# Kernel optimization log

Measured on AMD Instinct MI355X. Metric: run time of the kernel, lower is better.

Reference implementation:

```python
import jax, jax.numpy as jnp
import numpy as np

B, N = 2, 2048
DIM, NH, DH = 640, 10, 64
DINNER = 2560
L = 4
DEMB = 32
NTOKS = [128, 64]
NFEAT = 19
FDIM = 280
FEATD = DIM - DEMB * len(NTOKS)  # 576
SQRTD = float(np.sqrt(DH))


def _ln(x, g, b, eps=1e-5):
    m = jnp.mean(x, -1, keepdims=True)
    v = jnp.var(x, -1, keepdims=True)
    return (x - m) * jax.lax.rsqrt(v + eps) * g + b


def setup_inputs() -> dict:
    key = jax.random.key(0)
    ks = iter(jax.random.split(key, 32))
    s = 0.05
    return {
        "x_feats": jax.random.normal(next(ks), (B, N, NFEAT), jnp.float32),
        "x_toks": jax.random.randint(next(ks), (B, N, 2), 0, 64),
        "mask": jnp.ones((B, N), jnp.float32),
        "emb0": jax.random.normal(next(ks), (NTOKS[0] + 1, DEMB)) * s,
        "emb1": jax.random.normal(next(ks), (NTOKS[1] + 1, DEMB)) * s,
        "feat_w": jax.random.normal(next(ks), (FEATD, NFEAT)) * s,
        "feat_b": jnp.zeros((FEATD,)),
        "qkv_w": jax.random.normal(next(ks), (L, 3 * DIM, DIM)) * s,
        "qkv_b": jnp.zeros((L, 3 * DIM)),
        "o_w": jax.random.normal(next(ks), (L, DIM, DIM)) * s,
        "ln1_g": jnp.ones((L, DIM)), "ln1_b": jnp.zeros((L, DIM)),
        "ln2_g": jnp.ones((L, DIM)), "ln2_b": jnp.zeros((L, DIM)),
        "p1_w": jax.random.normal(next(ks), (L, DINNER, DIM)) * s,
        "p1_b": jnp.zeros((L, DINNER)),
        "p2_w": jax.random.normal(next(ks), (L, DIM, DINNER)) * s,
        "p2_b": jnp.zeros((L, DIM)),
        "fn_g": jnp.ones((DIM,)), "fn_b": jnp.zeros((DIM,)),
        "lin1_w": jax.random.normal(next(ks), (FDIM, DIM)) * s,
        "lin1_b": jnp.zeros((FDIM,)),
        "rb1_w": jax.random.normal(next(ks), (FDIM, FDIM)) * s,
        "rb1_b": jnp.zeros((FDIM,)),
        "rb2_w": jax.random.normal(next(ks), (FDIM, FDIM)) * s,
        "rb2_b": jnp.zeros((FDIM,)),
        "out_w": jax.random.normal(next(ks), (1, FDIM)) * s,
        "out_b": jnp.zeros((1,)),
    }


def _forward(x_feats, x_toks, mask, emb0, emb1, feat_w, feat_b,
             qkv_w, qkv_b, o_w, ln1_g, ln1_b, ln2_g, ln2_b,
             p1_w, p1_b, p2_w, p2_b, fn_g, fn_b,
             lin1_w, lin1_b, rb1_w, rb1_b, rb2_w, rb2_b, out_w, out_b):
    # mask outer product [B,N,N]; additive mask 0 where allowed, -1e20 elsewhere
    mask2 = jnp.einsum('bi,bj->bij', mask, mask)
    add_mask = jnp.where(mask2 > 0, 0.0, -1e20)

    # embeddings + feature projection -> [B,N,DIM]
    Z = jnp.concatenate([emb0[x_toks[..., 0]], emb1[x_toks[..., 1]],
                         x_feats @ feat_w.T + feat_b], axis=-1)

    def layer(Z, prm):
        qw, qb, ow, g1, b1, g2, b2, w1, c1, w2, c2 = prm
        inp = Z
        Zn = _ln(Z, g1, b1)
        # qkv reshaped to [B,N,H,3*DH], chunked along last dim: V, Q, K
        qkv = (Zn @ qw.T + qb).reshape(B, N, NH, 3 * DH)
        V, Q, K = qkv[..., :DH], qkv[..., DH:2 * DH], qkv[..., 2 * DH:]
        W = jnp.einsum('bnhd,bmhd->bhnm', Q, K) / SQRTD + add_mask[:, None]
        W = jax.nn.softmax(W, axis=3) * mask2[:, None]  # post-softmax mult mask
        attn = jnp.einsum('bhnm,bmhd->bnhd', W, V).reshape(B, N, DIM)
        Z = jax.nn.leaky_relu(attn) @ ow.T + inp  # leaky_relu BEFORE o_net
        inp = Z
        Zn = _ln(Z, g2, b2)
        Z = jax.nn.relu(Zn @ w1.T + c1) @ w2.T + c2 + inp
        return Z, None

    Z, _ = jax.lax.scan(layer, Z,
                        (qkv_w, qkv_b, o_w, ln1_g, ln1_b, ln2_g, ln2_b,
                         p1_w, p1_b, p2_w, p2_b))
    Z = _ln(Z, fn_g, fn_b)
    # ranking head: 1x1 convs == per-token linears
    h = Z @ lin1_w.T + lin1_b
    h = h + (jax.nn.relu(h @ rb1_w.T + rb1_b) @ rb2_w.T + rb2_b)
    return (h @ out_w.T + out_b)[..., 0]  # [B,N]


def reference(x_feats, x_toks, mask, emb0, emb1, feat_w, feat_b,
              qkv_w, qkv_b, o_w, ln1_g, ln1_b, ln2_g, ln2_b,
              p1_w, p1_b, p2_w, p2_b, fn_g, fn_b,
              lin1_w, lin1_b, rb1_w, rb1_b, rb2_w, rb2_b, out_w, out_b):
    return _forward(x_feats, x_toks, mask, emb0, emb1, feat_w, feat_b,
                    qkv_w, qkv_b, o_w, ln1_g, ln1_b, ln2_g, ln2_b,
                    p1_w, p1_b, p2_w, p2_b, fn_g, fn_b,
                    lin1_w, lin1_b, rb1_w, rb1_b, rb2_w, rb2_b, out_w, out_b)
```

## Files before the change

### kernel.cpp

```cpp
#include <hip/hip_runtime.h>

#define B_ 2
#define N_ 2048
#define DIM_ 640
#define NH_ 10
#define DH_ 64
#define DINNER_ 2560
#define L_ 4
#define FDIM_ 280
#define FDIMP_ 320
#define FEATD_ 576
#define NFEAT_ 19
#define ROWS_ (B_*N_)
#define NSPLIT_ 4
#define NITS_ 8

typedef __attribute__((ext_vector_type(8))) unsigned short ushort8;
typedef __attribute__((ext_vector_type(8))) __bf16 bf16x8;
typedef __attribute__((ext_vector_type(4))) __bf16 bf16x4;
typedef __attribute__((ext_vector_type(4))) float f32x4;
typedef __attribute__((ext_vector_type(2))) unsigned int u32x2;

static __device__ __forceinline__ unsigned short f2bf(float f){
  unsigned int u = __builtin_bit_cast(unsigned int, f);
  u += 0x7fffu + ((u >> 16) & 1u);
  return (unsigned short)(u >> 16);
}

static __device__ __forceinline__ f32x4 mfma16(ushort8 a, ushort8 b, f32x4 c){
  return __builtin_amdgcn_mfma_f32_16x16x32_bf16(
      __builtin_bit_cast(bf16x8, a), __builtin_bit_cast(bf16x8, b), c, 0, 0, 0);
}

#define GLD(src,dst) __builtin_amdgcn_global_load_lds((const __attribute__((address_space(1))) void*)(src), (__attribute__((address_space(3))) void*)(dst), 16, 0, 0)

#define SEG0 4915200
#define SEG1 1638400
#define SEG2 6553600
#define SEG3 6553600
#define SEG4 179200
#define SEG5 89600
#define SEG6 89600
#define SEG7 655360
#define SEG8 655360
#define SEG9 4096
#define E0 SEG0
#define E9 (SEG0+SEG1+SEG2+SEG3+SEG4+SEG5+SEG6+SEG7+SEG8+SEG9)

__global__ __launch_bounds__(256) void prep_kernel(
    const float* __restrict__ qkv_w, const float* __restrict__ o_w,
    const float* __restrict__ p1_w, const float* __restrict__ p2_w,
    const float* __restrict__ lin1_w, const float* __restrict__ rb1_w,
    const float* __restrict__ rb2_w, const float* __restrict__ mask,
    unsigned short* __restrict__ qkvw, unsigned short* __restrict__ oww,
    unsigned short* __restrict__ p1w, unsigned short* __restrict__ p2w,
    unsigned short* __restrict__ l1w, unsigned short* __restrict__ r1w,
    unsigned short* __restrict__ r2w, unsigned int* __restrict__ hb1z,
    unsigned int* __restrict__ hb2z, float* __restrict__ mbb)
{
  for (int i = blockIdx.x*256 + threadIdx.x; i < E9; i += gridDim.x*256){
    int j = i;
    if (j < E0) { qkvw[j] = f2bf(qkv_w[j]); continue; }
    j -= E0;
    if (j < SEG1) { oww[j] = f2bf(o_w[j]); continue; }
    j -= SEG1;
    if (j < SEG2) { p1w[j] = f2bf(p1_w[j]); continue; }
    j -= SEG2;
    if (j < SEG3) { p2w[j] = f2bf(p2_w[j]); continue; }
    j -= SEG3;
    if (j < SEG4) { l1w[j] = f2bf(lin1_w[j]); continue; }
    j -= SEG4;
    if (j < SEG5) { int r = j/FDIMP_, c = j - r*FDIMP_;
                    r1w[j] = (c<FDIM_) ? f2bf(rb1_w[r*FDIM_+c]) : (unsigned short)0; continue; }
    j -= SEG5;
    if (j < SEG6) { int r = j/FDIMP_, c = j - r*FDIMP_;
                    r2w[j] = (c<FDIM_) ? f2bf(rb2_w[r*FDIM_+c]) : (unsigned short)0; continue; }
    j -= SEG6;
    if (j < SEG7) { hb1z[j] = 0u; continue; }
    j -= SEG7;
    if (j < SEG8) { hb2z[j] = 0u; continue; }
    j -= SEG8;
    mbb[j] = (mask[j] > 0.f) ? 0.f : -1e30f;
  }
}

__global__ __launch_bounds__(256) void embed_kernel(const float* __restrict__ xf,
    const int* __restrict__ xt, const float* __restrict__ e0, const float* __restrict__ e1,
    const float* __restrict__ fw, const float* __restrict__ fb, float* __restrict__ Z){
  int row = blockIdx.x;
  __shared__ float f[NFEAT_];
  int t = threadIdx.x;
  if (t < NFEAT_) f[t] = xf[row*NFEAT_ + t];
  __syncthreads();
  if (t < 32) {
    int tok0 = xt[row*2];
    Z[(size_t)row*DIM_ + t] = e0[tok0*32 + t];
  } else if (t < 64) {
    int tok1 = xt[row*2+1];
    Z[(size_t)row*DIM_ + t] = e1[tok1*32 + (t-32)];
  }
  for (int fo = t; fo < FEATD_; fo += 256){
    float acc = fb[fo];
    #pragma unroll
    for (int k=0;k<NFEAT_;k++) acc += f[k]*fw[fo*NFEAT_+k];
    Z[(size_t)row*DIM_ + 64 + fo] = acc;
  }
}

__global__ __launch_bounds__(256) void ln_kernel(const float* __restrict__ X,
    const float* __restrict__ g, const float* __restrict__ bb,
    unsigned short* __restrict__ out){
  int lane = threadIdx.x & 63;
  int row = blockIdx.x*4 + (threadIdx.x >> 6);
  const float* x = X + (size_t)row*DIM_;
  float v[10]; float s=0.f, sq=0.f;
  #pragma unroll
  for (int j=0;j<10;j++){ float t = x[lane + j*64]; v[j]=t; s+=t; sq+=t*t; }
  #pragma unroll
  for (int off=1; off<64; off<<=1){ s += __shfl_xor(s, off, 64); sq += __shfl_xor(sq, off, 64); }
  float mean = s*(1.f/DIM_);
  float var = sq*(1.f/DIM_) - mean*mean;
  float rstd = rsqrtf(var + 1e-5f);
  unsigned short* o = out + (size_t)row*DIM_;
  #pragma unroll
  for (int j=0;j<10;j++){ int c = lane + j*64; o[c] = f2bf((v[j]-mean)*rstd*g[c] + bb[c]); }
}

template<bool BIAS, bool RELU, bool RES, bool OUTF, bool OUTB>
__global__ __launch_bounds__(256) void gemm_kernel(
    const unsigned short* __restrict__ A, int lda,
    const unsigned short* __restrict__ Bw, int ldb,
    const float* __restrict__ bias,
    const float* __restrict__ Res, int ldres,
    float* __restrict__ Cf, int ldcf,
    unsigned short* __restrict__ Cb, int ldcb,
    int Ncols, int K)
{
  __shared__ __align__(128) unsigned short As[2][8192];
  __shared__ __align__(128) unsigned short Bs[2][8192];
  int t = threadIdx.x;
  int wid = t >> 6, lane = t & 63;
  int wr = wid >> 1, wc = wid & 1;
  int lg = lane >> 4, lm = lane & 15;
  int orig = blockIdx.y*gridDim.x + blockIdx.x;
  int nwg = gridDim.x*gridDim.y;
  int wg = ((orig & 7) * (nwg >> 3)) + (orig >> 3);
  int bx = wg % gridDim.x, by = wg / gridDim.x;
  int row0 = by * 128;
  int col0 = bx * 128;

  const unsigned short* aSrc[4];
  const unsigned short* bSrc[4];
  #pragma unroll
  for (int j=0;j<4;j++){
    int s = t + j*256;
    int r = s >> 3;
    int c = (s & 7) ^ (((r >> 2) & 1) << 1);
    aSrc[j] = A + (size_t)(row0 + r)*lda + c*8;
    int br = col0 + r; if (br >= Ncols) br = Ncols - 1;
    bSrc[j] = Bw + (size_t)br*ldb + c*8;
  }

  f32x4 acc[4][4];
  #pragma unroll
  for (int m=0;m<4;m++)
    #pragma unroll
    for (int n=0;n<4;n++) acc[m][n] = f32x4{0.f,0.f,0.f,0.f};

  int nk = K >> 6;
  #pragma unroll
  for (int j=0;j<4;j++){
    GLD(aSrc[j], &As[0][(t + j*256)*8]);
    GLD(bSrc[j], &Bs[0][(t + j*256)*8]);
  }

  int swz = (lm & 4) >> 1;
  for (int tk=0; tk<nk; ++tk){
    int cur = tk & 1;
    if (tk+1 < nk){
      int kt = (tk+1) << 6;
      #pragma unroll
      for (int j=0;j<4;j++){
        GLD(aSrc[j]+kt, &As[cur^1][(t + j*256)*8]);
        GLD(bSrc[j]+kt, &Bs[cur^1][(t + j*256)*8]);
      }
      asm volatile("s_waitcnt vmcnt(8)" ::: "memory");
    } else {
      asm volatile("s_waitcnt vmcnt(0)" ::: "memory");
    }
    __builtin_amdgcn_s_barrier();
    asm volatile("" ::: "memory");
    const unsigned short* Ac = &As[cur][0];
    const unsigned short* Bc = &Bs[cur][0];
    #pragma unroll
    for (int kk=0;kk<2;kk++){
      int ch = ((kk*4 + lg) ^ swz) * 8;
      ushort8 af[4], bfr[4];
      #pragma unroll
      for (int m=0;m<4;m++) af[m] = *(const ushort8*)(Ac + (wr*64 + m*16 + lm)*64 + ch);
      #pragma unroll
      for (int n=0;n<4;n++) bfr[n] = *(const ushort8*)(Bc + (wc*64 + n*16 + lm)*64 + ch);
      #pragma unroll
      for (int m=0;m<4;m++)
        #pragma unroll
        for (int n=0;n<4;n++)
          acc[m][n] = mfma16(af[m], bfr[n], acc[m][n]);
    }
    asm volatile("" ::: "memory");
    __builtin_amdgcn_s_barrier();
  }

  #pragma unroll
  for (int m=0;m<4;m++){
    int rbase = row0 + wr*64 + m*16 + lg*4;
    #pragma unroll
    for (int n=0;n<4;n++){
      int cc = col0 + wc*64 + n*16 + lm;
      if (cc < Ncols){
        float bv = 0.f;
        if (BIAS) bv = bias[cc];
        #pragma unroll
        for (int rr=0;rr<4;rr++){
          float v = acc[m][n][rr] + bv;
          if (RELU) v = fmaxf(v, 0.f);
          if (RES) v += Res[(size_t)(rbase+rr)*ldres + cc];
          if (OUTF) Cf[(size_t)(rbase+rr)*ldcf + cc] = v;
          if (OUTB) Cb[(size_t)(rbase+rr)*ldcb + cc] = f2bf(v);
        }
      }
    }
  }
}

template<bool BIAS, bool RELU, bool RES, bool OUTF, bool OUTB>
__global__ __launch_bounds__(256) void gemm64_kernel(
    const unsigned short* __restrict__ A, int lda,
    const unsigned short* __restrict__ Bw, int ldb,
    const float* __restrict__ bias,
    const float* __restrict__ Res, int ldres,
    float* __restrict__ Cf, int ldcf,
    unsigned short* __restrict__ Cb, int ldcb,
    int Ncols, int K)
{
  __shared__ __align__(128) unsigned short As[2][64*64];
  __shared__ __align__(128) unsigned short Bs[2][64*64];
  int t = threadIdx.x;
  int wid = t >> 6, lane = t & 63;
  int wr = wid >> 1, wc = wid & 1;
  int lg = lane >> 4, lm = lane & 15;
  int orig = blockIdx.y*gridDim.x + blockIdx.x;
  int nwg = gridDim.x*gridDim.y;
  int wg = ((orig & 7) * (nwg >> 3)) + (orig >> 3);
  int bx = wg % gridDim.x, by = wg / gridDim.x;
  int row0 = by * 64;
  int col0 = bx * 64;

  int ar0 = t >> 3;
  int ar1 = ar0 + 32;
  int aq = (t & 7) ^ (((ar0 >> 2) & 1) << 1);
  const unsigned short* a0 = A + (size_t)(row0+ar0)*lda + aq*8;
  const unsigned short* a1 = A + (size_t)(row0+ar1)*lda + aq*8;
  int br0 = col0+ar0; if (br0 >= Ncols) br0 = Ncols-1;
  int br1 = col0+ar1; if (br1 >= Ncols) br1 = Ncols-1;
  const unsigned short* b0 = Bw + (size_t)br0*ldb + aq*8;
  const unsigned short* b1 = Bw + (size_t)br1*ldb + aq*8;
  int l0 = t*8, l1 = (t+256)*8;

  f32x4 acc[2][2];
  #pragma unroll
  for (int m=0;m<2;m++)
    #pragma unroll
    for (int n=0;n<2;n++) acc[m][n] = f32x4{0.f,0.f,0.f,0.f};

  int nk = K >> 6;
  GLD(a0, &As[0][l0]); GLD(b0, &Bs[0][l0]);
  GLD(a1, &As[0][l1]); GLD(b1, &Bs[0][l1]);

  int swz = (lm & 4) >> 1;
  for (int tk=0; tk<nk; ++tk){
    int cur = tk & 1;
    if (tk+1 < nk){
      int koff = (tk+1) << 6;
      GLD(a0+koff, &As[cur^1][l0]); GLD(b0+koff, &Bs[cur^1][l0]);
      GLD(a1+koff, &As[cur^1][l1]); GLD(b1+koff, &Bs[cur^1][l1]);
      asm volatile("s_waitcnt vmcnt(4)" ::: "memory");
    } else {
      asm volatile("s_waitcnt vmcnt(0)" ::: "memory");
    }
    __builtin_amdgcn_s_barrier();
    asm volatile("" ::: "memory");
    const unsigned short* Ac = &As[cur][0];
    const unsigned short* Bc = &Bs[cur][0];
    #pragma unroll
    for (int kk=0;kk<2;kk++){
      int ch = ((kk*4 + lg) ^ swz) * 8;
      ushort8 af[2], bfr[2];
      #pragma unroll
      for (int m=0;m<2;m++) af[m] = *(const ushort8*)(Ac + (wr*32 + m*16 + lm)*64 + ch);
      #pragma unroll
      for (int n=0;n<2;n++) bfr[n] = *(const ushort8*)(Bc + (wc*32 + n*16 + lm)*64 + ch);
      #pragma unroll
      for (int m=0;m<2;m++)
        #pragma unroll
        for (int n=0;n<2;n++)
          acc[m][n] = mfma16(af[m], bfr[n], acc[m][n]);
    }
    asm volatile("" ::: "memory");
    __builtin_amdgcn_s_barrier();
  }

  #pragma unroll
  for (int m=0;m<2;m++){
    int rbase = row0 + wr*32 + m*16 + lg*4;
    #pragma unroll
    for (int n=0;n<2;n++){
      int cc = col0 + wc*32 + n*16 + lm;
      if (cc < Ncols){
        float bv = 0.f;
        if (BIAS) bv = bias[cc];
        #pragma unroll
        for (int rr=0;rr<4;rr++){
          float v = acc[m][n][rr] + bv;
          if (RELU) v = fmaxf(v, 0.f);
          if (RES) v += Res[(size_t)(rbase+rr)*ldres + cc];
          if (OUTF) Cf[(size_t)(rbase+rr)*ldcf + cc] = v;
          if (OUTB) Cb[(size_t)(rbase+rr)*ldcb + cc] = f2bf(v);
        }
      }
    }
  }
}

__global__ __launch_bounds__(256) void attn_kernel(const unsigned short* __restrict__ qkv,
    const float* __restrict__ mb, unsigned short* __restrict__ op, float* __restrict__ lpp){
  int bh = blockIdx.y; int b = bh/NH_, h = bh%NH_;
  int t = threadIdx.x; int wid = t>>6, lane = t&63, lg = lane>>4, lm = lane&15;
  int q0 = blockIdx.x*64 + wid*16;
  int it0 = blockIdx.z * NITS_;
  size_t prow = (size_t)blockIdx.z*ROWS_ + b*N_;

  __shared__ __align__(128) unsigned short Ks[2][4096];
  __shared__ __align__(128) unsigned short Vs[2][4096];
  __shared__ __align__(16) float maskL[NITS_*64];

  const size_t base = (size_t)b*N_*1920 + (size_t)h*192;
  const size_t kvoff = (size_t)it0*64*1920;

  int c0 = t, c1 = t+256;
  int kk0 = c0>>3, kc0 = (c0&7)^(kk0&7);
  int kk1 = c1>>3, kc1 = (c1&7)^(kk1&7);
  const unsigned short* kS0 = qkv + base + kvoff + 128 + (size_t)kk0*1920 + kc0*8;
  const unsigned short* kS1 = qkv + base + kvoff + 128 + (size_t)kk1*1920 + kc1*8;
  int vk0 = ((c0>>5)<<2)|((c0>>1)&3), vd0 = (((c0>>3)&3)<<1)|(c0&1);
  int vk1 = ((c1>>5)<<2)|((c1>>1)&3), vd1 = (((c1>>3)&3)<<1)|(c1&1);
  const unsigned short* vS0 = qkv + base + kvoff + (size_t)vk0*1920 + vd0*8;
  const unsigned short* vS1 = qkv + base + kvoff + (size_t)vk1*1920 + vd1*8;

  ushort8 qf[2];
  #pragma unroll
  for (int ss=0; ss<2; ss++)
    qf[ss] = *(const ushort8*)(qkv + base + (size_t)(q0+lm)*1920 + 64 + ss*32 + lg*8);
  float cb2 = mb[b*N_ + q0 + lm] - 17.3123405f;

  if (t < 128) GLD(mb + b*N_ + it0*64 + t*4, &maskL[t*4]);
  GLD(kS0, &Ks[0][c0*8]); GLD(kS1, &Ks[0][c1*8]);
  GLD(vS0, &Vs[0][c0*8]); GLD(vS1, &Vs[0][c1*8]);

  float lp = 0.f;
  f32x4 o[4];
  #pragma unroll
  for (int dn=0;dn<4;dn++) o[dn] = f32x4{0.f,0.f,0.f,0.f};

  for (int ii=0; ii<NITS_; ++ii){
    int cur = ii & 1;
    if (ii < NITS_ - 1){
      const size_t adv = (size_t)(ii+1)*64*1920;
      GLD(kS0+adv, &Ks[1-cur][c0*8]); GLD(kS1+adv, &Ks[1-cur][c1*8]);
      GLD(vS0+adv, &Vs[1-cur][c0*8]); GLD(vS1+adv, &Vs[1-cur][c1*8]);
      asm volatile("s_waitcnt vmcnt(4)" ::: "memory");
    } else {
      asm volatile("s_waitcnt vmcnt(0)" ::: "memory");
    }
    __builtin_amdgcn_s_barrier();
    asm volatile("" ::: "memory");

    const unsigned short* Kc = &Ks[cur][0];
    f32x4 sf[4];
    #pragma unroll
    for (int c=0;c<4;c++){
      int krow = c*16 + lm;
      f32x4 s = f32x4{0.f,0.f,0.f,0.f};
      #pragma unroll
      for (int ss=0;ss<2;ss++){
        ushort8 kf = *(const ushort8*)(Kc + (krow*8 + ((ss*4+lg)^(krow&7)))*8);
        s = mfma16(kf, qf[ss], s);
      }
      sf[c] = s;
    }
    f32x4 mkv[4];
    #pragma unroll
    for (int c=0;c<4;c++) mkv[c] = *(const f32x4*)&maskL[ii*64 + c*16 + lg*4];

    unsigned vsb = (unsigned)(size_t)(__attribute__((address_space(3))) unsigned short*)&Vs[cur][0];
    unsigned a0 = vsb + lg*512 + lm*8;
    u32x2 vb[4][4];
    asm volatile(
      "ds_read_b64_tr_b16 %0, %4 offset:0\n\t"
      "ds_read_b64_tr_b16 %1, %4 offset:128\n\t"
      "ds_read_b64_tr_b16 %2, %4 offset:256\n\t"
      "ds_read_b64_tr_b16 %3, %4 offset:384"
      : "=&v"(vb[0][0]),"=&v"(vb[0][1]),"=&v"(vb[0][2]),"=&v"(vb[0][3]) : "v"(a0));
    asm volatile(
      "ds_read_b64_tr_b16 %0, %4 offset:2048\n\t"
      "ds_read_b64_tr_b16 %1, %4 offset:2176\n\t"
      "ds_read_b64_tr_b16 %2, %4 offset:2304\n\t"
      "ds_read_b64_tr_b16 %3, %4 offset:2432"
      : "=&v"(vb[1][0]),"=&v"(vb[1][1]),"=&v"(vb[1][2]),"=&v"(vb[1][3]) : "v"(a0));
    asm volatile(
      "ds_read_b64_tr_b16 %0, %4 offset:4096\n\t"
      "ds_read_b64_tr_b16 %1, %4 offset:4224\n\t"
      "ds_read_b64_tr_b16 %2, %4 offset:4352\n\t"
      "ds_read_b64_tr_b16 %3, %4 offset:4480"
      : "=&v"(vb[2][0]),"=&v"(vb[2][1]),"=&v"(vb[2][2]),"=&v"(vb[2][3]) : "v"(a0));
    asm volatile(
      "ds_read_b64_tr_b16 %0, %4 offset:6144\n\t"
      "ds_read_b64_tr_b16 %1, %4 offset:6272\n\t"
      "ds_read_b64_tr_b16 %2, %4 offset:6400\n\t"
      "ds_read_b64_tr_b16 %3, %4 offset:6528"
      : "=&v"(vb[3][0]),"=&v"(vb[3][1]),"=&v"(vb[3][2]),"=&v"(vb[3][3]) : "v"(a0));

    float pm[4][4]; bf16x4 pa[4];
    #pragma unroll
    for (int c=0;c<4;c++){
      #pragma unroll
      for (int r=0;r<4;r++){
        float x = fmaf(sf[c][r], 0.18033688f, cb2 + mkv[c][r]);
        pm[c][r] = __builtin_amdgcn_exp2f(x);
      }
      lp += (pm[c][0]+pm[c][1]) + (pm[c][2]+pm[c][3]);
      pa[c] = bf16x4{(__bf16)pm[c][0], (__bf16)pm[c][1], (__bf16)pm[c][2], (__bf16)pm[c][3]};
    }

#define PVM(dn_, c_) asm("v_mfma_f32_16x16x16_bf16 %0, %1, %2, %0" \
      : "+v"(o[dn_]) : "v"(__builtin_bit_cast(u32x2, pa[c_])), "v"(vb[c_][dn_]))
    asm volatile("s_waitcnt lgkmcnt(8)" ::: "memory");
    __builtin_amdgcn_sched_barrier(0);
    __builtin_amdgcn_s_setprio(1);
    PVM(0,0); PVM(1,0); PVM(2,0); PVM(3,0);
    PVM(0,1); PVM(1,1); PVM(2,1); PVM(3,1);
    asm volatile("s_waitcnt lgkmcnt(0)" ::: "memory");
    __builtin_amdgcn_sched_barrier(0);
    PVM(0,2); PVM(1,2); PVM(2,2); PVM(3,2);
    PVM(0,3); PVM(1,3); PVM(2,3); PVM(3,3);
    __builtin_amdgcn_s_setprio(0);
#undef PVM
    asm volatile("" ::: "memory");
    __builtin_amdgcn_s_barrier();
  }

  float s = lp;
  s += __shfl_xor(s, 16, 64);
  s += __shfl_xor(s, 32, 64);
  if (lg == 0) lpp[(prow + q0 + lm)*NH_ + h] = s;
  #pragma unroll
  for (int r=0;r<4;r++){
    unsigned short* ob = op + (prow + q0 + lg*4 + r)*DIM_ + h*64;
    #pragma unroll
    for (int dn=0;dn<4;dn++)
      ob[dn*16 + lm] = f2bf(o[dn][r]);
  }
}

__global__ __launch_bounds__(256) void attnred_kernel(const unsigned short* __restrict__ op,
    const float* __restrict__ lpp, unsigned short* __restrict__ att){
  int idx = blockIdx.x*256 + threadIdx.x;
  int row = idx / 80;
  int c8 = (idx - row*80) * 8;
  int h = c8 >> 6;
  float l = 0.f;
  #pragma unroll
  for (int s=0;s<NSPLIT_;s++) l += lpp[((size_t)s*ROWS_ + row)*NH_ + h];
  float inv = 1.0f / fmaxf(l, 1e-30f);
  float acc[8] = {0.f,0.f,0.f,0.f,0.f,0.f,0.f,0.f};
  #pragma unroll
  for (int s=0;s<NSPLIT_;s++){
    ushort8 v = *(const ushort8*)(op + ((size_t)s*ROWS_ + row)*DIM_ + c8);
    #pragma unroll
    for (int j=0;j<8;j++) acc[j] += __builtin_bit_cast(float, (unsigned)v[j] << 16);
  }
  ushort8 rr;
  #pragma unroll
  for (int j=0;j<8;j++){
    float v = acc[j] * inv;
    v = (v >= 0.f) ? v : 0.01f*v;
    rr[j] = f2bf(v);
  }
  *(ushort8*)(att + (size_t)row*DIM_ + c8) = rr;
}

__global__ __launch_bounds__(256) void out_kernel(const float* __restrict__ hf,
    const float* __restrict__ ow, const float* __restrict__ ob, float* __restrict__ out){
  int lane = threadIdx.x & 63;
  int row = blockIdx.x*4 + (threadIdx.x>>6);
  const float* x = hf + (size_t)row*FDIM_;
  float s = 0.f;
  for (int j=lane;j<FDIM_;j+=64) s += x[j]*ow[j];
  #pragma unroll
  for (int off=1; off<64; off<<=1) s += __shfl_xor(s, off, 64);
  if (lane==0) out[row] = s + ob[0];
}

extern "C" void kernel_launch(void* const* d_in, const int* in_sizes, int n_in,
                              void* d_out, int out_size, void* d_ws, size_t ws_size,
                              hipStream_t stream)
{
  const float* x_feats = (const float*)d_in[0];
  const int*   x_toks  = (const int*)d_in[1];
  const float* mask    = (const float*)d_in[2];
  const float* emb0    = (const float*)d_in[3];
  const float* emb1    = (const float*)d_in[4];
  const float* feat_w  = (const float*)d_in[5];
  const float* feat_b  = (const float*)d_in[6];
  const float* qkv_w   = (const float*)d_in[7];
  const float* qkv_b   = (const float*)d_in[8];
  const float* o_w     = (const float*)d_in[9];
  const float* ln1_g   = (const float*)d_in[10];
  const float* ln1_b   = (const float*)d_in[11];
  const float* ln2_g   = (const float*)d_in[12];
  const float* ln2_b   = (const float*)d_in[13];
  const float* p1_w    = (const float*)d_in[14];
  const float* p1_b    = (const float*)d_in[15];
  const float* p2_w    = (const float*)d_in[16];
  const float* p2_b    = (const float*)d_in[17];
  const float* fn_g    = (const float*)d_in[18];
  const float* fn_b    = (const float*)d_in[19];
  const float* lin1_w  = (const float*)d_in[20];
  const float* lin1_b  = (const float*)d_in[21];
  const float* rb1_w   = (const float*)d_in[22];
  const float* rb1_b   = (const float*)d_in[23];
  const float* rb2_w   = (const float*)d_in[24];
  const float* rb2_b   = (const float*)d_in[25];
  const float* out_w   = (const float*)d_in[26];
  const float* out_b   = (const float*)d_in[27];
  float* out = (float*)d_out;

  char* w = (char*)d_ws;
  auto alloc = [&](size_t bytes)->void*{ void* p = (void*)w; w += (bytes + 255) & ~(size_t)255; return p; };

  float* Z              = (float*)alloc((size_t)ROWS_*DIM_*4);
  unsigned short* Zn    = (unsigned short*)alloc((size_t)ROWS_*DIM_*2);
  unsigned short* qkvB  = (unsigned short*)alloc((size_t)ROWS_*1920*2);
  unsigned short* attB  = (unsigned short*)alloc((size_t)ROWS_*DIM_*2);
  unsigned short* Hb    = (unsigned short*)alloc((size_t)ROWS_*DINNER_*2);
  float* hf             = (float*)alloc((size_t)ROWS_*FDIM_*4);
  unsigned short* hb1   = (unsigned short*)alloc((size_t)ROWS_*FDIMP_*2);
  unsigned short* hb2   = (unsigned short*)alloc((size_t)ROWS_*FDIMP_*2);
  float* mbb            = (float*)alloc((size_t)ROWS_*4);
  unsigned short* opart = (unsigned short*)alloc((size_t)NSPLIT_*ROWS_*DIM_*2);
  float* lpart          = (float*)alloc((size_t)NSPLIT_*ROWS_*NH_*4);
  unsigned short* qkvw  = (unsigned short*)alloc((size_t)L_*1920*DIM_*2);
  unsigned short* oww   = (unsigned short*)alloc((size_t)L_*DIM_*DIM_*2);
  unsigned short* p1w   = (unsigned short*)alloc((size_t)L_*DINNER_*DIM_*2);
  unsigned short* p2w   = (unsigned short*)alloc((size_t)L_*DIM_*DINNER_*2);
  unsigned short* l1w   = (unsigned short*)alloc((size_t)FDIM_*DIM_*2);
  unsigned short* r1w   = (unsigned short*)alloc((size_t)FDIM_*FDIMP_*2);
  unsigned short* r2w   = (unsigned short*)alloc((size_t)FDIM_*FDIMP_*2);

  prep_kernel<<<2048,256,0,stream>>>(qkv_w, o_w, p1_w, p2_w, lin1_w, rb1_w, rb2_w, mask,
      qkvw, oww, p1w, p2w, l1w, r1w, r2w,
      (unsigned int*)hb1, (unsigned int*)hb2, mbb);

  embed_kernel<<<ROWS_,256,0,stream>>>(x_feats, x_toks, emb0, emb1, feat_w, feat_b, Z);

  for (int l=0; l<L_; l++){
    ln_kernel<<<ROWS_/4,256,0,stream>>>(Z, ln1_g + l*DIM_, ln1_b + l*DIM_, Zn);
    gemm_kernel<true,false,false,false,true><<<dim3(15,32),256,0,stream>>>(
        Zn, DIM_, qkvw + (size_t)l*1920*DIM_, DIM_, qkv_b + l*1920,
        nullptr, 0, nullptr, 0, qkvB, 1920, 1920, DIM_);
    attn_kernel<<<dim3(N_/64, B_*NH_, NSPLIT_),256,0,stream>>>(qkvB, mbb, opart, lpart);
    attnred_kernel<<<ROWS_*80/256,256,0,stream>>>(opart, lpart, attB);
    gemm64_kernel<false,false,true,true,false><<<dim3(10,64),256,0,stream>>>(
        attB, DIM_, oww + (size_t)l*DIM_*DIM_, DIM_, nullptr,
        Z, DIM_, Z, DIM_, nullptr, 0, DIM_, DIM_);
    ln_kernel<<<ROWS_/4,256,0,stream>>>(Z, ln2_g + l*DIM_, ln2_b + l*DIM_, Zn);
    gemm_kernel<true,true,false,false,true><<<dim3(20,32),256,0,stream>>>(
        Zn, DIM_, p1w + (size_t)l*DINNER_*DIM_, DIM_, p1_b + l*DINNER_,
        nullptr, 0, nullptr, 0, Hb, DINNER_, DINNER_, DIM_);
    gemm64_kernel<true,false,true,true,false><<<dim3(10,64),256,0,stream>>>(
        Hb, DINNER_, p2w + (size_t)l*DIM_*DINNER_, DINNER_, p2_b + l*DIM_,
        Z, DIM_, Z, DIM_, nullptr, 0, DIM_, DINNER_);
  }

  ln_kernel<<<ROWS_/4,256,0,stream>>>(Z, fn_g, fn_b, Zn);
  gemm64_kernel<true,false,false,true,true><<<dim3(5,64),256,0,stream>>>(
      Zn, DIM_, l1w, DIM_, lin1_b, nullptr, 0, hf, FDIM_, hb1, FDIMP_, FDIM_, DIM_);
  gemm64_kernel<true,true,false,false,true><<<dim3(5,64),256,0,stream>>>(
      hb1, FDIMP_, r1w, FDIMP_, rb1_b, nullptr, 0, nullptr, 0, hb2, FDIMP_, FDIM_, FDIMP_);
  gemm64_kernel<true,false,true,true,false><<<dim3(5,64),256,0,stream>>>(
      hb2, FDIMP_, r2w, FDIMP_, rb2_b, hf, FDIM_, hf, FDIM_, nullptr, 0, FDIM_, FDIMP_);
  out_kernel<<<ROWS_/4,256,0,stream>>>(hf, out_w, out_b, out);
}
```

Measured before the change: 640.8 us.

## Halve attention KV tile to 32 keys and vectorize prep conversions

The attention kernel now streams 32-key K/V tiles instead of 64-key tiles over 16 iterations, which halves the LDS footprint and the per-iteration register arrays (scores, V fragments, probabilities). The intent is higher occupancy and lower register pressure, at the cost of more barriers and loop iterations per block. Separately, the prep kernel converts and zeroes four elements per thread with vector loads and stores to cut instruction count in the one-time weight conversion.

```diff
diff --git a/kernel.cpp b/kernel.cpp
--- a/kernel.cpp
+++ b/kernel.cpp
@@ -13,9 +13,11 @@
 #define NFEAT_ 19
 #define ROWS_ (B_*N_)
 #define NSPLIT_ 4
-#define NITS_ 8
+#define NT2_ 16
 
 typedef __attribute__((ext_vector_type(8))) unsigned short ushort8;
+typedef __attribute__((ext_vector_type(4))) unsigned short ushort4v;
+typedef __attribute__((ext_vector_type(4))) unsigned int u32x4;
 typedef __attribute__((ext_vector_type(8))) __bf16 bf16x8;
 typedef __attribute__((ext_vector_type(4))) __bf16 bf16x4;
 typedef __attribute__((ext_vector_type(4))) float f32x4;
@@ -25,6 +27,13 @@
   unsigned int u = __builtin_bit_cast(unsigned int, f);
   u += 0x7fffu + ((u >> 16) & 1u);
   return (unsigned short)(u >> 16);
+}
+
+static __device__ __forceinline__ void cvt4(const float* __restrict__ s, unsigned short* __restrict__ d){
+  f32x4 v = *(const f32x4*)s;
+  ushort4v r;
+  r[0]=f2bf(v[0]); r[1]=f2bf(v[1]); r[2]=f2bf(v[2]); r[3]=f2bf(v[3]);
+  *(ushort4v*)d = r;
 }
 
 static __device__ __forceinline__ f32x4 mfma16(ushort8 a, ushort8 b, f32x4 c){
@@ -58,29 +67,41 @@
     unsigned short* __restrict__ r2w, unsigned int* __restrict__ hb1z,
     unsigned int* __restrict__ hb2z, float* __restrict__ mbb)
 {
-  for (int i = blockIdx.x*256 + threadIdx.x; i < E9; i += gridDim.x*256){
-    int j = i;
-    if (j < E0) { qkvw[j] = f2bf(qkv_w[j]); continue; }
+  for (int i = blockIdx.x*256 + threadIdx.x; i < E9/4; i += gridDim.x*256){
+    int j = i*4;
+    if (j < E0) { cvt4(qkv_w+j, qkvw+j); continue; }
     j -= E0;
-    if (j < SEG1) { oww[j] = f2bf(o_w[j]); continue; }
+    if (j < SEG1) { cvt4(o_w+j, oww+j); continue; }
     j -= SEG1;
-    if (j < SEG2) { p1w[j] = f2bf(p1_w[j]); continue; }
+    if (j < SEG2) { cvt4(p1_w+j, p1w+j); continue; }
     j -= SEG2;
-    if (j < SEG3) { p2w[j] = f2bf(p2_w[j]); continue; }
+    if (j < SEG3) { cvt4(p2_w+j, p2w+j); continue; }
     j -= SEG3;
-    if (j < SEG4) { l1w[j] = f2bf(lin1_w[j]); continue; }
+    if (j < SEG4) { cvt4(lin1_w+j, l1w+j); continue; }
     j -= SEG4;
-    if (j < SEG5) { int r = j/FDIMP_, c = j - r*FDIMP_;
-                    r1w[j] = (c<FDIM_) ? f2bf(rb1_w[r*FDIM_+c]) : (unsigned short)0; continue; }
+    if (j < SEG5) {
+      #pragma unroll
+      for (int e=0;e<4;e++){ int jj=j+e; int r=jj/FDIMP_, c=jj-r*FDIMP_;
+        r1w[jj] = (c<FDIM_) ? f2bf(rb1_w[r*FDIM_+c]) : (unsigned short)0; }
+      continue; }
     j -= SEG5;
-    if (j < SEG6) { int r = j/FDIMP_, c = j - r*FDIMP_;
-                    r2w[j] = (c<FDIM_) ? f2bf(rb2_w[r*FDIM_+c]) : (unsigned short)0; continue; }
+    if (j < SEG6) {
+      #pragma unroll
+      for (int e=0;e<4;e++){ int jj=j+e; int r=jj/FDIMP_, c=jj-r*FDIMP_;
+        r2w[jj] = (c<FDIM_) ? f2bf(rb2_w[r*FDIM_+c]) : (unsigned short)0; }
+      continue; }
     j -= SEG6;
-    if (j < SEG7) { hb1z[j] = 0u; continue; }
+    if (j < SEG7) { *(u32x4*)(hb1z+j) = u32x4{0u,0u,0u,0u}; continue; }
     j -= SEG7;
-    if (j < SEG8) { hb2z[j] = 0u; continue; }
+    if (j < SEG8) { *(u32x4*)(hb2z+j) = u32x4{0u,0u,0u,0u}; continue; }
     j -= SEG8;
-    mbb[j] = (mask[j] > 0.f) ? 0.f : -1e30f;
+    {
+      f32x4 m = *(const f32x4*)(mask+j);
+      f32x4 r;
+      #pragma unroll
+      for (int e=0;e<4;e++) r[e] = (m[e] > 0.f) ? 0.f : -1e30f;
+      *(f32x4*)(mbb+j) = r;
+    }
   }
 }
 
@@ -336,25 +357,20 @@
   int bh = blockIdx.y; int b = bh/NH_, h = bh%NH_;
   int t = threadIdx.x; int wid = t>>6, lane = t&63, lg = lane>>4, lm = lane&15;
   int q0 = blockIdx.x*64 + wid*16;
-  int it0 = blockIdx.z * NITS_;
+  int k0 = blockIdx.z * (NT2_*32);
   size_t prow = (size_t)blockIdx.z*ROWS_ + b*N_;
 
-  __shared__ __align__(128) unsigned short Ks[2][4096];
-  __shared__ __align__(128) unsigned short Vs[2][4096];
-  __shared__ __align__(16) float maskL[NITS_*64];
+  __shared__ __align__(128) unsigned short Ks[2][2048];
+  __shared__ __align__(128) unsigned short Vs[2][2048];
+  __shared__ __align__(16) float maskL[NT2_*32];
 
   const size_t base = (size_t)b*N_*1920 + (size_t)h*192;
-  const size_t kvoff = (size_t)it0*64*1920;
-
-  int c0 = t, c1 = t+256;
-  int kk0 = c0>>3, kc0 = (c0&7)^(kk0&7);
-  int kk1 = c1>>3, kc1 = (c1&7)^(kk1&7);
+  const size_t kvoff = (size_t)k0*1920;
+
+  int kk0 = t>>3, kc0 = (t&7)^(kk0&7);
   const unsigned short* kS0 = qkv + base + kvoff + 128 + (size_t)kk0*1920 + kc0*8;
-  const unsigned short* kS1 = qkv + base + kvoff + 128 + (size_t)kk1*1920 + kc1*8;
-  int vk0 = ((c0>>5)<<2)|((c0>>1)&3), vd0 = (((c0>>3)&3)<<1)|(c0&1);
-  int vk1 = ((c1>>5)<<2)|((c1>>1)&3), vd1 = (((c1>>3)&3)<<1)|(c1&1);
+  int vk0 = ((t>>5)<<2)|((t>>1)&3), vd0 = (((t>>3)&3)<<1)|(t&1);
   const unsigned short* vS0 = qkv + base + kvoff + (size_t)vk0*1920 + vd0*8;
-  const unsigned short* vS1 = qkv + base + kvoff + (size_t)vk1*1920 + vd1*8;
 
   ushort8 qf[2];
   #pragma unroll
@@ -362,22 +378,22 @@
     qf[ss] = *(const ushort8*)(qkv + base + (size_t)(q0+lm)*1920 + 64 + ss*32 + lg*8);
   float cb2 = mb[b*N_ + q0 + lm] - 17.3123405f;
 
-  if (t < 128) GLD(mb + b*N_ + it0*64 + t*4, &maskL[t*4]);
-  GLD(kS0, &Ks[0][c0*8]); GLD(kS1, &Ks[0][c1*8]);
-  GLD(vS0, &Vs[0][c0*8]); GLD(vS1, &Vs[0][c1*8]);
+  if (t < 128) GLD(mb + b*N_ + k0 + t*4, &maskL[t*4]);
+  GLD(kS0, &Ks[0][t*8]);
+  GLD(vS0, &Vs[0][t*8]);
 
   float lp = 0.f;
   f32x4 o[4];
   #pragma unroll
   for (int dn=0;dn<4;dn++) o[dn] = f32x4{0.f,0.f,0.f,0.f};
 
-  for (int ii=0; ii<NITS_; ++ii){
+  for (int ii=0; ii<NT2_; ++ii){
     int cur = ii & 1;
-    if (ii < NITS_ - 1){
-      const size_t adv = (size_t)(ii+1)*64*1920;
-      GLD(kS0+adv, &Ks[1-cur][c0*8]); GLD(kS1+adv, &Ks[1-cur][c1*8]);
-      GLD(vS0+adv, &Vs[1-cur][c0*8]); GLD(vS1+adv, &Vs[1-cur][c1*8]);
-      asm volatile("s_waitcnt vmcnt(4)" ::: "memory");
+    if (ii < NT2_ - 1){
+      const size_t adv = (size_t)(ii+1)*32*1920;
+      GLD(kS0+adv, &Ks[1-cur][t*8]);
+      GLD(vS0+adv, &Vs[1-cur][t*8]);
+      asm volatile("s_waitcnt vmcnt(2)" ::: "memory");
     } else {
       asm volatile("s_waitcnt vmcnt(0)" ::: "memory");
     }
@@ -385,9 +401,9 @@
     asm volatile("" ::: "memory");
 
     const unsigned short* Kc = &Ks[cur][0];
-    f32x4 sf[4];
-    #pragma unroll
-    for (int c=0;c<4;c++){
+    f32x4 sf[2];
+    #pragma unroll
+    for (int c=0;c<2;c++){
       int krow = c*16 + lm;
       f32x4 s = f32x4{0.f,0.f,0.f,0.f};
       #pragma unroll
@@ -397,13 +413,13 @@
       }
       sf[c] = s;
     }
-    f32x4 mkv[4];
-    #pragma unroll
-    for (int c=0;c<4;c++) mkv[c] = *(const f32x4*)&maskL[ii*64 + c*16 + lg*4];
+    f32x4 mkv[2];
+    #pragma unroll
+    for (int c=0;c<2;c++) mkv[c] = *(const f32x4*)&maskL[ii*32 + c*16 + lg*4];
 
     unsigned vsb = (unsigned)(size_t)(__attribute__((address_space(3))) unsigned short*)&Vs[cur][0];
     unsigned a0 = vsb + lg*512 + lm*8;
-    u32x2 vb[4][4];
+    u32x2 vb[2][4];
     asm volatile(
       "ds_read_b64_tr_b16 %0, %4 offset:0\n\t"
       "ds_read_b64_tr_b16 %1, %4 offset:128\n\t"
@@ -416,22 +432,10 @@
       "ds_read_b64_tr_b16 %2, %4 offset:2304\n\t"
       "ds_read_b64_tr_b16 %3, %4 offset:2432"
       : "=&v"(vb[1][0]),"=&v"(vb[1][1]),"=&v"(vb[1][2]),"=&v"(vb[1][3]) : "v"(a0));
-    asm volatile(
-      "ds_read_b64_tr_b16 %0, %4 offset:4096\n\t"
-      "ds_read_b64_tr_b16 %1, %4 offset:4224\n\t"
-      "ds_read_b64_tr_b16 %2, %4 offset:4352\n\t"
-      "ds_read_b64_tr_b16 %3, %4 offset:4480"
-      : "=&v"(vb[2][0]),"=&v"(vb[2][1]),"=&v"(vb[2][2]),"=&v"(vb[2][3]) : "v"(a0));
-    asm volatile(
-      "ds_read_b64_tr_b16 %0, %4 offset:6144\n\t"
-      "ds_read_b64_tr_b16 %1, %4 offset:6272\n\t"
-      "ds_read_b64_tr_b16 %2, %4 offset:6400\n\t"
-      "ds_read_b64_tr_b16 %3, %4 offset:6528"
-      : "=&v"(vb[3][0]),"=&v"(vb[3][1]),"=&v"(vb[3][2]),"=&v"(vb[3][3]) : "v"(a0));
-
-    float pm[4][4]; bf16x4 pa[4];
-    #pragma unroll
-    for (int c=0;c<4;c++){
+
+    float pm[2][4]; bf16x4 pa[2];
+    #pragma unroll
+    for (int c=0;c<2;c++){
       #pragma unroll
       for (int r=0;r<4;r++){
         float x = fmaf(sf[c][r], 0.18033688f, cb2 + mkv[c][r]);
@@ -443,15 +447,13 @@
 
 #define PVM(dn_, c_) asm("v_mfma_f32_16x16x16_bf16 %0, %1, %2, %0" \
       : "+v"(o[dn_]) : "v"(__builtin_bit_cast(u32x2, pa[c_])), "v"(vb[c_][dn_]))
-    asm volatile("s_waitcnt lgkmcnt(8)" ::: "memory");
+    asm volatile("s_waitcnt lgkmcnt(4)" ::: "memory");
     __builtin_amdgcn_sched_barrier(0);
     __builtin_amdgcn_s_setprio(1);
     PVM(0,0); PVM(1,0); PVM(2,0); PVM(3,0);
-    PVM(0,1); PVM(1,1); PVM(2,1); PVM(3,1);
     asm volatile("s_waitcnt lgkmcnt(0)" ::: "memory");
     __builtin_amdgcn_sched_barrier(0);
-    PVM(0,2); PVM(1,2); PVM(2,2); PVM(3,2);
-    PVM(0,3); PVM(1,3); PVM(2,3); PVM(3,3);
+    PVM(0,1); PVM(1,1); PVM(2,1); PVM(3,1);
     __builtin_amdgcn_s_setprio(0);
 #undef PVM
     asm volatile("" ::: "memory");
```

Measured after the change: 639.5 us. No clear change (-0.2%).
